# Optimization experiments

Measured on AMD Instinct MI355X. Metric: run time of the kernel, lower is better.

## Reference

```python
import jax, jax.numpy as jnp
import numpy as np

# LIF neuron constants (standard mem_update)
THRESH = 0.5
LENS = 0.5
DECAY = 0.25
EPS = 1e-5
NUM_HEADS = 8

@jax.custom_vjp
def act_fun(mem):
    return (mem > THRESH).astype(mem.dtype)

def _act_fwd(mem):
    return act_fun(mem), mem

def _act_bwd(mem, g):
    surrogate = (jnp.abs(mem - THRESH) < LENS).astype(g.dtype)
    return (g * surrogate,)

act_fun.defvjp(_act_fwd, _act_bwd)

def mem_update(x):
    # x: (T, ...) -> binary spikes (T, ...) via recurrent LIF dynamics
    def step(carry, xt):
        mem_old, spike = carry
        # spike is detached in the reset gate (torch .detach())
        mem = mem_old * DECAY * (1.0 - jax.lax.stop_gradient(spike)) + xt
        s = act_fun(mem)
        return (mem, s), s
    init = (jnp.zeros_like(x[0]), jnp.zeros_like(x[0]))
    _, out = jax.lax.scan(step, init, x)
    return out

def bn(x, gamma, beta, mean, var):
    # inference-mode BatchNorm1d over channel dim of (T,B,C,L)
    inv = gamma / jnp.sqrt(var + EPS)
    return x * inv[None, None, :, None] + (beta - mean * inv)[None, None, :, None]

def setup_inputs() -> dict:
    key = jax.random.key(0)
    ks = jax.random.split(key, 11)
    T, B, C, L = 4, 2, 384, 1024
    s = 1.0 / np.sqrt(C)
    return {
        "x": jax.random.normal(ks[0], (T, B, C, L), jnp.float32),
        "W_w": jax.random.normal(ks[1], (2 * C, C), jnp.float32) * s,
        "bn1_gamma": jax.random.uniform(ks[2], (2 * C,), jnp.float32, 0.5, 1.5),
        "bn1_beta": jax.random.normal(ks[3], (2 * C,), jnp.float32) * 0.1,
        "bn1_mean": jax.random.normal(ks[4], (2 * C,), jnp.float32) * 0.1,
        "bn1_var": jax.random.uniform(ks[5], (2 * C,), jnp.float32, 0.5, 1.5),
        "proj_w": jax.random.normal(ks[6], (C, C), jnp.float32) * s,
        "bn2_gamma": jax.random.uniform(ks[7], (C,), jnp.float32, 0.5, 1.5),
        "bn2_beta": jax.random.normal(ks[8], (C,), jnp.float32) * 0.1,
        "bn2_mean": jax.random.normal(ks[9], (C,), jnp.float32) * 0.1,
        "bn2_var": jax.random.uniform(ks[10], (C,), jnp.float32, 0.5, 1.5),
    }

def reference(x, W_w, bn1_gamma, bn1_beta, bn1_mean, bn1_var, proj_w, bn2_gamma, bn2_beta, bn2_mean, bn2_var):
    T, B, C, L = x.shape
    H = NUM_HEADS
    d = C // H
    x_feat = x
    xs = mem_update(x)                                   # binary spikes (T,B,C,L)
    y = jnp.einsum('oc,tbcl->tbol', W_w, xs)             # 1x1 conv C->2C
    y = bn(y, bn1_gamma, bn1_beta, bn1_mean, bn1_var)
    y = y.reshape(T, B, H, 2 * d, L)
    y1, y2 = y[:, :, :, :d, :], y[:, :, :, d:, :]
    xr = xs.reshape(T, B, H, d, L)
    attn = jnp.einsum('tbhdl,tbhdm->tbhlm', y1, xr)      # (L,L) per head
    attn = mem_update(attn)                              # binary spikes
    out = jnp.einsum('tbhdl,tbhlm->tbhdm', y2, attn)
    out = out.reshape(T, B, C, L)
    out = mem_update(out)
    out = jnp.einsum('oc,tbcl->tbol', proj_w, out)       # Wproj 1x1
    out = bn(out, bn2_gamma, bn2_beta, bn2_mean, bn2_var)
    return out + x_feat
```

## Files before the change

### kernel.cpp

```cpp
#include <hip/hip_runtime.h>

#define T_  4
#define B_  2
#define C_  384
#define L_  1024
#define H_  8
#define C2_ 768
#define S_  (B_*C_*L_)

typedef __attribute__((ext_vector_type(8))) short short8;
typedef __attribute__((ext_vector_type(4))) float floatx4;
typedef __attribute__((ext_vector_type(16))) float floatx16;

__device__ __forceinline__ unsigned bf16_rne(float v) {
    unsigned u = __float_as_uint(v);
    u += 0x7FFFu + ((u >> 16) & 1u);
    return u >> 16;
}
__device__ __forceinline__ float bf16_to_f(unsigned h) { return __uint_as_float(h << 16); }
__device__ __forceinline__ void split3(float v, unsigned& hi, unsigned& mi, unsigned& lo) {
    hi = bf16_rne(v);
    float r1 = v - bf16_to_f(hi);
    mi = bf16_rne(r1);
    float r2 = r1 - bf16_to_f(mi);
    lo = bf16_rne(r2);
}

__global__ __launch_bounds__(256) void scan_and_split(
    const float* __restrict__ src, unsigned short* __restrict__ dstT,
    const float* __restrict__ Wa, int n4a,
    unsigned short* __restrict__ hia, unsigned short* __restrict__ mia,
    unsigned short* __restrict__ loa,
    const float* __restrict__ Wb, int n4b,
    unsigned short* __restrict__ hib, unsigned short* __restrict__ mib,
    unsigned short* __restrict__ lob) {
    __shared__ unsigned short tile[64][72];
    const int tid = threadIdx.x;
    if (blockIdx.x >= 192) {
        int i = (blockIdx.x - 192) * 256 + tid;
        const float* W; unsigned short *hi, *mi, *lo;
        if (i < n4a) { W = Wa; hi = hia; mi = mia; lo = loa; }
        else {
            i -= n4a;
            if (i >= n4b) return;
            W = Wb; hi = hib; mi = mib; lo = lob;
        }
        float4 v = ((const float4*)W)[i];
        float vv[4] = {v.x, v.y, v.z, v.w};
        union { unsigned short us[4]; uint2 u2; } h, m, l;
#pragma unroll
        for (int e = 0; e < 4; e++) {
            unsigned hh, mm, ll; split3(vv[e], hh, mm, ll);
            h.us[e] = (unsigned short)hh; m.us[e] = (unsigned short)mm; l.us[e] = (unsigned short)ll;
        }
        ((uint2*)hi)[i] = h.u2; ((uint2*)mi)[i] = m.u2; ((uint2*)lo)[i] = l.u2;
        return;
    }
    const int job = blockIdx.x;
    const int l0 = (job & 15) * 64;
    const int c0 = ((job >> 4) % 6) * 64;
    const int b  = job / 96;
    const int row = tid >> 2, seg = tid & 3;
    float mem[16], sp[16];
#pragma unroll
    for (int e = 0; e < 16; e++) { mem[e] = 0.f; sp[e] = 0.f; }
    for (int t = 0; t < T_; t++) {
        const size_t base = ((size_t)((t*B_ + b)*C_ + c0 + row))*L_ + l0 + seg*16;
#pragma unroll
        for (int qq = 0; qq < 4; qq++) {
            float4 v = *(const float4*)(src + base + qq*4);
            float vv[4] = {v.x, v.y, v.z, v.w};
            unsigned bs[4];
#pragma unroll
            for (int s = 0; s < 4; s++) {
                int e = qq*4 + s;
                mem[e] = mem[e]*0.25f*(1.f - sp[e]) + vv[s];
                bool sb = mem[e] > 0.5f;
                sp[e] = sb ? 1.f : 0.f;
                bs[s] = sb ? 0x3F80u : 0u;
            }
            *(unsigned*)&tile[row][seg*16 + qq*4]     = bs[0] | (bs[1] << 16);
            *(unsigned*)&tile[row][seg*16 + qq*4 + 2] = bs[2] | (bs[3] << 16);
        }
        __syncthreads();
        {
            const int lr = tid >> 2, cs = tid & 3;
#pragma unroll
            for (int sub = 0; sub < 2; sub++) {
                unsigned wv[4];
#pragma unroll
                for (int p = 0; p < 4; p++) {
                    unsigned e0 = tile[cs*16 + sub*8 + p*2][lr];
                    unsigned e1 = tile[cs*16 + sub*8 + p*2 + 1][lr];
                    wv[p] = e0 | (e1 << 16);
                }
                uint4 o; o.x = wv[0]; o.y = wv[1]; o.z = wv[2]; o.w = wv[3];
                *(uint4*)(dstT + ((size_t)(t*B_ + b)*L_ + l0 + lr)*C_ + c0 + cs*16 + sub*8) = o;
            }
        }
        __syncthreads();
    }
}

__global__ __launch_bounds__(256) void scan_transpose(const float* __restrict__ src,
                                                      unsigned short* __restrict__ dstT) {
    __shared__ unsigned short tile[64][72];
    const int tid = threadIdx.x;
    const int l0 = blockIdx.x * 64, c0 = blockIdx.y * 64, b = blockIdx.z;
    const int row = tid >> 2, seg = tid & 3;
    float mem[16], sp[16];
#pragma unroll
    for (int e = 0; e < 16; e++) { mem[e] = 0.f; sp[e] = 0.f; }
    for (int t = 0; t < T_; t++) {
        const size_t base = ((size_t)((t*B_ + b)*C_ + c0 + row))*L_ + l0 + seg*16;
#pragma unroll
        for (int qq = 0; qq < 4; qq++) {
            float4 v = *(const float4*)(src + base + qq*4);
            float vv[4] = {v.x, v.y, v.z, v.w};
            unsigned bs[4];
#pragma unroll
            for (int s = 0; s < 4; s++) {
                int e = qq*4 + s;
                mem[e] = mem[e]*0.25f*(1.f - sp[e]) + vv[s];
                bool sb = mem[e] > 0.5f;
                sp[e] = sb ? 1.f : 0.f;
                bs[s] = sb ? 0x3F80u : 0u;
            }
            *(unsigned*)&tile[row][seg*16 + qq*4]     = bs[0] | (bs[1] << 16);
            *(unsigned*)&tile[row][seg*16 + qq*4 + 2] = bs[2] | (bs[3] << 16);
        }
        __syncthreads();
        {
            const int lr = tid >> 2, cs = tid & 3;
#pragma unroll
            for (int sub = 0; sub < 2; sub++) {
                unsigned wv[4];
#pragma unroll
                for (int p = 0; p < 4; p++) {
                    unsigned e0 = tile[cs*16 + sub*8 + p*2][lr];
                    unsigned e1 = tile[cs*16 + sub*8 + p*2 + 1][lr];
                    wv[p] = e0 | (e1 << 16);
                }
                uint4 o; o.x = wv[0]; o.y = wv[1]; o.z = wv[2]; o.w = wv[3];
                *(uint4*)(dstT + ((size_t)(t*B_ + b)*L_ + l0 + lr)*C_ + c0 + cs*16 + sub*8) = o;
            }
        }
        __syncthreads();
    }
}

__global__ __launch_bounds__(256) void gemm1_mfma(
    const unsigned short* __restrict__ whi, const unsigned short* __restrict__ wmi,
    const unsigned short* __restrict__ wlo, const unsigned short* __restrict__ xsT,
    const float* __restrict__ g, const float* __restrict__ be,
    const float* __restrict__ mn, const float* __restrict__ vr,
    unsigned short* __restrict__ y1hi, unsigned short* __restrict__ y1mi,
    unsigned short* __restrict__ y1lo,
    unsigned short* __restrict__ y2hi, unsigned short* __restrict__ y2mi,
    unsigned short* __restrict__ y2lo) {
    __shared__ unsigned short smem[14080];
    const int tid = threadIdx.x;
    const int flat = blockIdx.x;
    const int tb = flat & 7;
    const int ii = flat >> 3;
    const int mt = ii >> 4, lt = ii & 15;
    const int l0 = lt * 64;
    const int w = tid >> 6, lane = tid & 63;
    const int q = lane >> 4, n15 = lane & 15;
    const int mw = (w & 1) * 48, lw = (w >> 1) * 32;

    floatx4 acc[3][2];
#pragma unroll
    for (int i = 0; i < 3; i++)
#pragma unroll
        for (int j = 0; j < 2; j++) acc[i][j] = (floatx4){0.f,0.f,0.f,0.f};

    for (int ck = 0; ck < C_; ck += 32) {
#pragma unroll
        for (int p = 0; p < 3; p++) {
            const unsigned short* wp = p == 0 ? whi : p == 1 ? wmi : wlo;
            unsigned short* ap = smem + p*3840;
            for (int s = tid; s < 384; s += 256) {
                int r = s >> 2, c = s & 3;
                *(uint4*)&ap[r*40 + c*8] = *(const uint4*)(wp + (size_t)(mt*96 + r)*C_ + ck + c*8);
            }
        }
        {
            int r = tid >> 2, c = tid & 3;
            *(uint4*)&smem[11520 + r*40 + c*8] =
                *(const uint4*)(xsT + ((size_t)tb*L_ + l0 + r)*C_ + ck + c*8);
        }
        __syncthreads();
        short8 bb[2];
#pragma unroll
        for (int in = 0; in < 2; in++)
            bb[in] = *(short8*)&smem[11520 + (lw + in*16 + n15)*40 + q*8];
#pragma unroll
        for (int im = 0; im < 3; im++) {
            short8 ah = *(short8*)&smem[       (mw + im*16 + n15)*40 + q*8];
            short8 am = *(short8*)&smem[3840 + (mw + im*16 + n15)*40 + q*8];
            short8 al = *(short8*)&smem[7680 + (mw + im*16 + n15)*40 + q*8];
#pragma unroll
            for (int in = 0; in < 2; in++) {
                acc[im][in] = __builtin_amdgcn_mfma_f32_16x16x32_bf16(ah, bb[in], acc[im][in], 0,0,0);
                acc[im][in] = __builtin_amdgcn_mfma_f32_16x16x32_bf16(am, bb[in], acc[im][in], 0,0,0);
                acc[im][in] = __builtin_amdgcn_mfma_f32_16x16x32_bf16(al, bb[in], acc[im][in], 0,0,0);
            }
        }
        __syncthreads();
    }

#pragma unroll
    for (int im = 0; im < 3; im++)
#pragma unroll
        for (int r = 0; r < 4; r++) {
            int o = mt*96 + mw + im*16 + q*4 + r;
            float inv = g[o] / sqrtf(vr[o] + 1e-5f);
            float sh = be[o] - mn[o]*inv;
#pragma unroll
            for (int in = 0; in < 2; in++)
                acc[im][in][r] = acc[im][in][r]*inv + sh;
        }
    const bool isY1 = ((w & 1) == 0);
#pragma unroll
    for (int p = 0; p < 3; p++) {
        if (isY1) {
#pragma unroll
            for (int im = 0; im < 3; im++)
#pragma unroll
                for (int in = 0; in < 2; in++) {
                    union { unsigned short us[4]; uint2 u2; } pk;
#pragma unroll
                    for (int r = 0; r < 4; r++) {
                        unsigned hh = bf16_rne(acc[im][in][r]);
                        pk.us[r] = (unsigned short)hh;
                        acc[im][in][r] -= bf16_to_f(hh);
                    }
                    *(uint2*)&smem[(lw + in*16 + n15)*56 + im*16 + q*4] = pk.u2;
                }
        } else {
#pragma unroll
            for (int im = 0; im < 3; im++)
#pragma unroll
                for (int in = 0; in < 2; in++)
#pragma unroll
                    for (int r = 0; r < 4; r++) {
                        unsigned hh = bf16_rne(acc[im][in][r]);
                        smem[3584 + (im*16 + q*4 + r)*72 + lw + in*16 + n15] = (unsigned short)hh;
                        acc[im][in][r] -= bf16_to_f(hh);
                    }
        }
        __syncthreads();
        unsigned short* y1p = p == 0 ? y1hi : p == 1 ? y1mi : y1lo;
        unsigned short* y2p = p == 0 ? y2hi : p == 1 ? y2mi : y2lo;
        for (int s = tid; s < 384; s += 256) {
            int r1 = s / 6, c8 = s % 6;
            *(uint4*)(y1p + (((size_t)tb*H_ + mt)*L_ + l0 + r1)*48 + c8*8) =
                *(uint4*)&smem[r1*56 + c8*8];
        }
        for (int s = tid; s < 384; s += 256) {
            int cr = s >> 3, lq = s & 7;
            *(uint4*)(y2p + ((size_t)tb*C_ + mt*48 + cr)*L_ + l0 + lq*8) =
                *(uint4*)&smem[3584 + cr*72 + lq*8];
        }
        __syncthreads();
    }
}

__global__ __launch_bounds__(256) void attn_spike_mfma(
    const unsigned short* __restrict__ y1hi, const unsigned short* __restrict__ y1mi,
    const unsigned short* __restrict__ y1lo, const unsigned short* __restrict__ xsT,
    unsigned* __restrict__ bits) {
    __shared__ unsigned short A_hi[64][56], A_mi[64][56], A_lo[64][56], B_s[128][56];
    __shared__ unsigned bits_s[128][2];
    const int tid = threadIdx.x;
    const int flat = blockIdx.x;
    const int xcd = flat & 7;
    const int ii = flat >> 3;
    const int bh = xcd*2 + (ii >> 7);
    const int rr = ii & 127;
    const int b = bh >> 3, h = bh & 7;
    const int lbase = (rr >> 3) * 64;
    const int mbase = (rr & 7) * 128;
    const int w = tid >> 6, lane = tid & 63;
    const int l31 = lane & 31, half = lane >> 5;

    float mem[2][16];
#pragma unroll
    for (int il = 0; il < 2; il++)
#pragma unroll
        for (int r = 0; r < 16; r++) mem[il][r] = 0.f;

    for (int t = 0; t < T_; t++) {
        const int tb = t*B_ + b;
        const size_t yb = (((size_t)tb*H_ + h)*L_ + lbase)*48;
        const size_t xb = ((size_t)tb*L_ + mbase)*C_ + h*48;
        for (int s = tid; s < 384; s += 256) {
            int r = s / 6, c = s % 6;
            size_t ro = yb + (size_t)r*48 + c*8;
            *(uint4*)&A_hi[r][c*8] = *(const uint4*)(y1hi + ro);
            *(uint4*)&A_mi[r][c*8] = *(const uint4*)(y1mi + ro);
            *(uint4*)&A_lo[r][c*8] = *(const uint4*)(y1lo + ro);
        }
        for (int s = tid; s < 768; s += 256) {
            int r = s / 6, c = s % 6;
            *(uint4*)&B_s[r][c*8] = *(const uint4*)(xsT + xb + (size_t)r*C_ + c*8);
        }
        bits_s[tid >> 1][tid & 1] = 0u;
        __syncthreads();

        floatx16 acc[2];
#pragma unroll
        for (int il = 0; il < 2; il++)
#pragma unroll
            for (int r = 0; r < 16; r++) acc[il][r] = 0.f;

#pragma unroll
        for (int ks = 0; ks < 3; ks++) {
            const int kcol = ks*16 + half*8;
            short8 bb = *(short8*)&B_s[w*32 + l31][kcol];
#pragma unroll
            for (int il = 0; il < 2; il++) {
                short8 ah = *(short8*)&A_hi[il*32 + l31][kcol];
                short8 am = *(short8*)&A_mi[il*32 + l31][kcol];
                short8 al = *(short8*)&A_lo[il*32 + l31][kcol];
                acc[il] = __builtin_amdgcn_mfma_f32_32x32x16_bf16(ah, bb, acc[il], 0,0,0);
                acc[il] = __builtin_amdgcn_mfma_f32_32x32x16_bf16(am, bb, acc[il], 0,0,0);
                acc[il] = __builtin_amdgcn_mfma_f32_32x32x16_bf16(al, bb, acc[il], 0,0,0);
            }
        }

#pragma unroll
        for (int il = 0; il < 2; il++) {
            unsigned word = 0;
#pragma unroll
            for (int r = 0; r < 16; r++) {
                float m = (mem[il][r] > 0.5f ? 0.f : mem[il][r]*0.25f) + acc[il][r];
                mem[il][r] = m;
                int lloc = (r & 3) + 8*(r >> 2) + 4*half;
                word |= (m > 0.5f) ? (1u << lloc) : 0u;
            }
            atomicOr(&bits_s[w*32 + l31][il], word);
        }
        __syncthreads();
        {
            int m = tid >> 1, wd = tid & 1;
            bits[((size_t)(tb*H_ + h)*L_ + mbase + m)*32 + (lbase >> 5) + wd] = bits_s[m][wd];
        }
        __syncthreads();
    }
}

__global__ __launch_bounds__(256) void attn_out_mfma(
    const unsigned short* __restrict__ y2hi, const unsigned short* __restrict__ y2mi,
    const unsigned short* __restrict__ y2lo,
    const unsigned* __restrict__ bits, float* __restrict__ outpre) {
    __shared__ unsigned short A_hi[48][72], A_mi[48][72], A_lo[48][72];
    const int tid = threadIdx.x;
    const int flat = blockIdx.x;
    const int xcd = flat & 7;
    const int ii = flat >> 3;
    const int tbh = xcd*8 + (ii >> 3);
    const int mtile = ii & 7;
    const int t = tbh >> 4, b = (tbh >> 3) & 1, h = tbh & 7;
    const int tb = t*B_ + b;
    const int w = tid >> 6, lane = tid & 63;
    const int q = lane >> 4, n15 = lane & 15;
    const int mb = mtile*128 + w*32;

    floatx4 acc[3][2];
#pragma unroll
    for (int i = 0; i < 3; i++)
#pragma unroll
        for (int in = 0; in < 2; in++) acc[i][in] = (floatx4){0.f,0.f,0.f,0.f};

    const unsigned* brow0 = bits + ((size_t)(tb*H_ + h)*L_ + mb + n15)*32;
    const unsigned* brow1 = brow0 + 16*32;
    const size_t y2b = ((size_t)tb*C_ + h*48)*L_;

    for (int lt = 0; lt < L_; lt += 64) {
        for (int s = tid; s < 384; s += 256) {
            int r = s >> 3, c = s & 7;
            size_t ro = y2b + (size_t)r*L_ + lt + c*8;
            *(uint4*)&A_hi[r][c*8] = *(const uint4*)(y2hi + ro);
            *(uint4*)&A_mi[r][c*8] = *(const uint4*)(y2mi + ro);
            *(uint4*)&A_lo[r][c*8] = *(const uint4*)(y2lo + ro);
        }
        uint2 bw0 = *(const uint2*)(brow0 + (lt >> 5));
        uint2 bw1 = *(const uint2*)(brow1 + (lt >> 5));
        __syncthreads();
#pragma unroll
        for (int kc = 0; kc < 2; kc++) {
            unsigned word0 = kc ? bw0.y : bw0.x;
            unsigned word1 = kc ? bw1.y : bw1.x;
            unsigned byt0 = (word0 >> (q*8)) & 0xFFu;
            unsigned byt1 = (word1 >> (q*8)) & 0xFFu;
            union { unsigned u[4]; short8 v; } bu0, bu1;
#pragma unroll
            for (int p = 0; p < 4; p++) {
                bu0.u[p] = (((byt0 >> (2*p)) & 1u) ? 0x3F80u : 0u)
                         | (((byt0 >> (2*p+1)) & 1u) ? 0x3F800000u : 0u);
                bu1.u[p] = (((byt1 >> (2*p)) & 1u) ? 0x3F80u : 0u)
                         | (((byt1 >> (2*p+1)) & 1u) ? 0x3F800000u : 0u);
            }
            short8 bf0 = bu0.v, bf1 = bu1.v;
#pragma unroll
            for (int i = 0; i < 3; i++) {
                int ra = i*16 + n15;
                short8 ah = *(short8*)&A_hi[ra][kc*32 + q*8];
                short8 am = *(short8*)&A_mi[ra][kc*32 + q*8];
                short8 al = *(short8*)&A_lo[ra][kc*32 + q*8];
                acc[i][0] = __builtin_amdgcn_mfma_f32_16x16x32_bf16(ah, bf0, acc[i][0], 0,0,0);
                acc[i][0] = __builtin_amdgcn_mfma_f32_16x16x32_bf16(am, bf0, acc[i][0], 0,0,0);
                acc[i][0] = __builtin_amdgcn_mfma_f32_16x16x32_bf16(al, bf0, acc[i][0], 0,0,0);
                acc[i][1] = __builtin_amdgcn_mfma_f32_16x16x32_bf16(ah, bf1, acc[i][1], 0,0,0);
                acc[i][1] = __builtin_amdgcn_mfma_f32_16x16x32_bf16(am, bf1, acc[i][1], 0,0,0);
                acc[i][1] = __builtin_amdgcn_mfma_f32_16x16x32_bf16(al, bf1, acc[i][1], 0,0,0);
            }
        }
        __syncthreads();
    }
#pragma unroll
    for (int i = 0; i < 3; i++)
#pragma unroll
        for (int r = 0; r < 4; r++) {
            int d = i*16 + q*4 + r;
#pragma unroll
            for (int in = 0; in < 2; in++)
                outpre[((size_t)tb*C_ + h*48 + d)*L_ + mb + in*16 + n15] = acc[i][in][r];
        }
}

__global__ __launch_bounds__(256) void gemm2_mfma(
    const unsigned short* __restrict__ whi, const unsigned short* __restrict__ wmi,
    const unsigned short* __restrict__ wlo, const unsigned short* __restrict__ xT,
    const float* __restrict__ g, const float* __restrict__ be,
    const float* __restrict__ mn, const float* __restrict__ vr,
    const float* __restrict__ res, float* __restrict__ out) {
    __shared__ unsigned short A_hi[96][40], A_mi[96][40], A_lo[96][40];
    __shared__ unsigned short B_s[64][40];
    const int tid = threadIdx.x;
    const int tb = blockIdx.y;
    const int mt = blockIdx.x >> 4, lt = blockIdx.x & 15;
    const int l0 = lt * 64;
    const int w = tid >> 6, lane = tid & 63;
    const int q = lane >> 4, n15 = lane & 15;
    const int mw = (w & 1) * 48, lw = (w >> 1) * 32;

    floatx4 acc[3][2];
#pragma unroll
    for (int i = 0; i < 3; i++)
#pragma unroll
        for (int j = 0; j < 2; j++) acc[i][j] = (floatx4){0.f,0.f,0.f,0.f};

    for (int ck = 0; ck < C_; ck += 32) {
#pragma unroll
        for (int p = 0; p < 3; p++) {
            const unsigned short* wp = p == 0 ? whi : p == 1 ? wmi : wlo;
            unsigned short (*ap)[40] = p == 0 ? A_hi : p == 1 ? A_mi : A_lo;
            for (int s = tid; s < 384; s += 256) {
                int r = s >> 2, c = s & 3;
                *(uint4*)&ap[r][c*8] = *(const uint4*)(wp + (size_t)(mt*96 + r)*C_ + ck + c*8);
            }
        }
        {
            int r = tid >> 2, c4 = tid & 3;
            *(uint4*)&B_s[r][c4*8] = *(const uint4*)(xT + ((size_t)tb*L_ + l0 + r)*C_ + ck + c4*8);
        }
        __syncthreads();
        short8 bb[2];
#pragma unroll
        for (int in = 0; in < 2; in++)
            bb[in] = *(short8*)&B_s[lw + in*16 + n15][q*8];
#pragma unroll
        for (int im = 0; im < 3; im++) {
            short8 ah = *(short8*)&A_hi[mw + im*16 + n15][q*8];
            short8 am = *(short8*)&A_mi[mw + im*16 + n15][q*8];
            short8 al = *(short8*)&A_lo[mw + im*16 + n15][q*8];
#pragma unroll
            for (int in = 0; in < 2; in++) {
                acc[im][in] = __builtin_amdgcn_mfma_f32_16x16x32_bf16(ah, bb[in], acc[im][in], 0,0,0);
                acc[im][in] = __builtin_amdgcn_mfma_f32_16x16x32_bf16(am, bb[in], acc[im][in], 0,0,0);
                acc[im][in] = __builtin_amdgcn_mfma_f32_16x16x32_bf16(al, bb[in], acc[im][in], 0,0,0);
            }
        }
        __syncthreads();
    }
#pragma unroll
    for (int im = 0; im < 3; im++)
#pragma unroll
        for (int r = 0; r < 4; r++) {
            int o = mt*96 + mw + im*16 + q*4 + r;
            float inv = g[o] / sqrtf(vr[o] + 1e-5f);
            float sh = be[o] - mn[o]*inv;
#pragma unroll
            for (int in = 0; in < 2; in++) {
                int l = l0 + lw + in*16 + n15;
                size_t idx = ((size_t)tb*C_ + o)*L_ + l;
                out[idx] = acc[im][in][r]*inv + sh + res[idx];
            }
        }
}

extern "C" void kernel_launch(void* const* d_in, const int* in_sizes, int n_in,
                              void* d_out, int out_size, void* d_ws, size_t ws_size,
                              hipStream_t stream) {
    const float* x   = (const float*)d_in[0];
    const float* W_w = (const float*)d_in[1];
    const float* g1  = (const float*)d_in[2];
    const float* b1  = (const float*)d_in[3];
    const float* m1  = (const float*)d_in[4];
    const float* v1  = (const float*)d_in[5];
    const float* pw  = (const float*)d_in[6];
    const float* g2  = (const float*)d_in[7];
    const float* b2  = (const float*)d_in[8];
    const float* m2  = (const float*)d_in[9];
    const float* v2  = (const float*)d_in[10];

    float* ws = (float*)d_ws;
    unsigned short* xsT  = (unsigned short*)ws;
    unsigned short* y1hi = (unsigned short*)(ws + 1572864);
    unsigned short* y1mi = (unsigned short*)(ws + 3145728);
    unsigned short* y1lo = (unsigned short*)(ws + 4718592);
    unsigned short* y2hi = (unsigned short*)(ws + 6291456);
    unsigned short* y2mi = (unsigned short*)(ws + 7864320);
    unsigned short* y2lo = (unsigned short*)(ws + 9437184);
    unsigned*       bits = (unsigned*)(ws + 11010048);
    unsigned short* wspl[3]  = {(unsigned short*)(ws + 13107200),
                                (unsigned short*)(ws + 13254656),
                                (unsigned short*)(ws + 13402112)};
    unsigned short* pwspl[3] = {(unsigned short*)(ws + 13549568),
                                (unsigned short*)(ws + 13623296),
                                (unsigned short*)(ws + 13697024)};
    float*          outpre = (float*)(ws + 1572864);
    unsigned short* outsT  = (unsigned short*)(ws + 4718592);
    float* out = (float*)d_out;

    scan_and_split<<<dim3(624), 256, 0, stream>>>(x, xsT,
                                                  W_w, C2_*C_/4, wspl[0], wspl[1], wspl[2],
                                                  pw,  C_*C_/4, pwspl[0], pwspl[1], pwspl[2]);
    gemm1_mfma<<<dim3(1024), 256, 0, stream>>>(wspl[0], wspl[1], wspl[2], xsT,
                                               g1, b1, m1, v1,
                                               y1hi, y1mi, y1lo, y2hi, y2mi, y2lo);
    attn_spike_mfma<<<dim3(2048), 256, 0, stream>>>(y1hi, y1mi, y1lo, xsT, bits);
    attn_out_mfma<<<dim3(512), 256, 0, stream>>>(y2hi, y2mi, y2lo, bits, outpre);
    scan_transpose<<<dim3(16, 6, B_), 256, 0, stream>>>(outpre, outsT);
    gemm2_mfma<<<dim3(64, 8), 256, 0, stream>>>(pwspl[0], pwspl[1], pwspl[2], outsT,
                                                g2, b2, m2, v2, x, out);
}
```

Baseline: 222.5 us.

## Load attention-spike MFMA operands directly from global, drop LDS staging and barriers

The attn_spike kernel no longer stages the y1 hi/mi/lo tiles and the xs tile through shared memory. Each lane now loads its MFMA fragments straight from global memory, and the per-row spike bits are combined with a cross-half shuffle instead of LDS atomics. This removes every __syncthreads and all LDS traffic, and the launch bound is raised to 4 blocks per CU for occupancy. In exchange, each A tile is read from global or L2 by all four waves instead of once per block, and the short8 fragment loads are strided rather than coalesced.

New measurement: 227.4 us. +2.2%, slower.

```diff
diff --git a/kernel.cpp b/kernel.cpp
--- a/kernel.cpp
+++ b/kernel.cpp
@@ -267,12 +267,10 @@
     }
 }
 
-__global__ __launch_bounds__(256) void attn_spike_mfma(
+__global__ __launch_bounds__(256, 4) void attn_spike_mfma(
     const unsigned short* __restrict__ y1hi, const unsigned short* __restrict__ y1mi,
     const unsigned short* __restrict__ y1lo, const unsigned short* __restrict__ xsT,
     unsigned* __restrict__ bits) {
-    __shared__ unsigned short A_hi[64][56], A_mi[64][56], A_lo[64][56], B_s[128][56];
-    __shared__ unsigned bits_s[128][2];
     const int tid = threadIdx.x;
     const int flat = blockIdx.x;
     const int xcd = flat & 7;
@@ -284,6 +282,7 @@
     const int mbase = (rr & 7) * 128;
     const int w = tid >> 6, lane = tid & 63;
     const int l31 = lane & 31, half = lane >> 5;
+    const int mrow = mbase + w*32 + l31;
 
     float mem[2][16];
 #pragma unroll
@@ -293,21 +292,15 @@
 
     for (int t = 0; t < T_; t++) {
         const int tb = t*B_ + b;
-        const size_t yb = (((size_t)tb*H_ + h)*L_ + lbase)*48;
-        const size_t xb = ((size_t)tb*L_ + mbase)*C_ + h*48;
-        for (int s = tid; s < 384; s += 256) {
-            int r = s / 6, c = s % 6;
-            size_t ro = yb + (size_t)r*48 + c*8;
-            *(uint4*)&A_hi[r][c*8] = *(const uint4*)(y1hi + ro);
-            *(uint4*)&A_mi[r][c*8] = *(const uint4*)(y1mi + ro);
-            *(uint4*)&A_lo[r][c*8] = *(const uint4*)(y1lo + ro);
-        }
-        for (int s = tid; s < 768; s += 256) {
-            int r = s / 6, c = s % 6;
-            *(uint4*)&B_s[r][c*8] = *(const uint4*)(xsT + xb + (size_t)r*C_ + c*8);
-        }
-        bits_s[tid >> 1][tid & 1] = 0u;
-        __syncthreads();
+        const unsigned short* ya_hi = y1hi + (((size_t)tb*H_ + h)*L_ + lbase)*48;
+        const unsigned short* ya_mi = y1mi + (((size_t)tb*H_ + h)*L_ + lbase)*48;
+        const unsigned short* ya_lo = y1lo + (((size_t)tb*H_ + h)*L_ + lbase)*48;
+        const unsigned short* xrow  = xsT + ((size_t)tb*L_ + mrow)*C_ + h*48;
+
+        short8 bb[3];
+#pragma unroll
+        for (int ks = 0; ks < 3; ks++)
+            bb[ks] = *(const short8*)(xrow + ks*16 + half*8);
 
         floatx16 acc[2];
 #pragma unroll
@@ -318,18 +311,19 @@
 #pragma unroll
         for (int ks = 0; ks < 3; ks++) {
             const int kcol = ks*16 + half*8;
-            short8 bb = *(short8*)&B_s[w*32 + l31][kcol];
 #pragma unroll
             for (int il = 0; il < 2; il++) {
-                short8 ah = *(short8*)&A_hi[il*32 + l31][kcol];
-                short8 am = *(short8*)&A_mi[il*32 + l31][kcol];
-                short8 al = *(short8*)&A_lo[il*32 + l31][kcol];
-                acc[il] = __builtin_amdgcn_mfma_f32_32x32x16_bf16(ah, bb, acc[il], 0,0,0);
-                acc[il] = __builtin_amdgcn_mfma_f32_32x32x16_bf16(am, bb, acc[il], 0,0,0);
-                acc[il] = __builtin_amdgcn_mfma_f32_32x32x16_bf16(al, bb, acc[il], 0,0,0);
-            }
-        }
-
+                const int aoff = (il*32 + l31)*48 + kcol;
+                short8 ah = *(const short8*)(ya_hi + aoff);
+                short8 am = *(const short8*)(ya_mi + aoff);
+                short8 al = *(const short8*)(ya_lo + aoff);
+                acc[il] = __builtin_amdgcn_mfma_f32_32x32x16_bf16(ah, bb[ks], acc[il], 0,0,0);
+                acc[il] = __builtin_amdgcn_mfma_f32_32x32x16_bf16(am, bb[ks], acc[il], 0,0,0);
+                acc[il] = __builtin_amdgcn_mfma_f32_32x32x16_bf16(al, bb[ks], acc[il], 0,0,0);
+            }
+        }
+
+        unsigned wds[2];
 #pragma unroll
         for (int il = 0; il < 2; il++) {
             unsigned word = 0;
@@ -340,14 +334,14 @@
                 int lloc = (r & 3) + 8*(r >> 2) + 4*half;
                 word |= (m > 0.5f) ? (1u << lloc) : 0u;
             }
-            atomicOr(&bits_s[w*32 + l31][il], word);
-        }
-        __syncthreads();
-        {
-            int m = tid >> 1, wd = tid & 1;
-            bits[((size_t)(tb*H_ + h)*L_ + mbase + m)*32 + (lbase >> 5) + wd] = bits_s[m][wd];
-        }
-        __syncthreads();
+            wds[il] = word;
+        }
+        unsigned f0 = wds[0] | __shfl_xor(wds[0], 32);
+        unsigned f1 = wds[1] | __shfl_xor(wds[1], 32);
+        if (half == 0) {
+            uint2 o; o.x = f0; o.y = f1;
+            *(uint2*)(bits + ((size_t)(tb*H_ + h)*L_ + mrow)*32 + (lbase >> 5)) = o;
+        }
     }
 }
 
```
